# Kernel tuning notes

Hardware: AMD Instinct MI355X
Metric: run time of the kernel (lower is better)

The kernel has to match this reference:

```python
import jax, jax.numpy as jnp
import numpy as np

DIM = 2048
DIM_HEAD = 64
HEADS = 16
FF_MULT = 4
LORA_R = 8
ATTN_INNER = DIM_HEAD * HEADS            # 1024
FF_INNER = DIM * FF_MULT                 # 8192
FUSED_DIMS = (ATTN_INNER, DIM_HEAD, DIM_HEAD, FF_INNER * 2)
B, N = 2, 2048


def setup_inputs() -> dict:
    key = jax.random.key(0)
    ks = jax.random.split(key, 12)
    s = 0.02
    inp = {
        "x": jax.random.normal(ks[0], (B, N, DIM), dtype=jnp.float32),
        "gamma": jnp.ones((DIM,), dtype=jnp.float32),
        "w_fused": jax.random.normal(ks[1], (DIM, sum(FUSED_DIMS)), dtype=jnp.float32) * s,
        "w_attn_out": jax.random.normal(ks[2], (ATTN_INNER, DIM), dtype=jnp.float32) * s,
        "w_ff_out": jax.random.normal(ks[3], (FF_INNER, DIM), dtype=jnp.float32) * s,
        "lora_q_a": jax.random.normal(ks[4], (DIM, LORA_R), dtype=jnp.float32) * s,
        "lora_q_b": jax.random.normal(ks[5], (LORA_R, ATTN_INNER), dtype=jnp.float32) * s,
        "lora_k_a": jax.random.normal(ks[6], (DIM, LORA_R), dtype=jnp.float32) * s,
        "lora_k_b": jax.random.normal(ks[7], (LORA_R, DIM_HEAD), dtype=jnp.float32) * s,
        "lora_v_a": jax.random.normal(ks[8], (DIM, LORA_R), dtype=jnp.float32) * s,
        "lora_v_b": jax.random.normal(ks[9], (LORA_R, DIM_HEAD), dtype=jnp.float32) * s,
        "lora_o_a": jax.random.normal(ks[10], (ATTN_INNER, LORA_R), dtype=jnp.float32) * s,
        "lora_o_b": jax.random.normal(ks[11], (LORA_R, DIM), dtype=jnp.float32) * s,
    }
    return inp


def _rotate_half(x):
    x1, x2 = jnp.split(x, 2, axis=-1)
    return jnp.concatenate((-x2, x1), axis=-1)


def _rope(pos, t):
    return t * jnp.cos(pos) + _rotate_half(t) * jnp.sin(pos)


def _forward(x, gamma, w_fused, w_attn_out, w_ff_out,
             lora_q_a, lora_q_b, lora_k_a, lora_k_b,
             lora_v_a, lora_v_b, lora_o_a, lora_o_b):
    b, n, d = x.shape
    # LayerNorm (beta = 0)
    mu = jnp.mean(x, axis=-1, keepdims=True)
    var = jnp.var(x, axis=-1, keepdims=True)
    xn = (x - mu) * jax.lax.rsqrt(var + 1e-5) * gamma

    fused = xn @ w_fused
    i0, i1, i2 = np.cumsum(FUSED_DIMS)[:3]
    q, k, v, ff = fused[..., :i0], fused[..., i0:i1], fused[..., i1:i2], fused[..., i2:]

    # LoRA additive terms
    q = q + (xn @ lora_q_a) @ lora_q_b
    k = k + (xn @ lora_k_a) @ lora_k_b
    v = v + (xn @ lora_v_a) @ lora_v_b

    q = q.reshape(b, n, HEADS, DIM_HEAD).transpose(0, 2, 1, 3)  # b h n d
    q = q * (DIM_HEAD ** -0.5)

    # rotary embedding: pos (n, dim_head)
    inv_freq = 1.0 / (10000.0 ** (jnp.arange(0, DIM_HEAD, 2, dtype=jnp.float32) / DIM_HEAD))
    freqs = jnp.arange(n, dtype=jnp.float32)[:, None] * inv_freq[None, :]
    pos = jnp.concatenate((freqs, freqs), axis=-1)
    q = _rope(pos, q)
    k = _rope(pos, k)  # k is b n d (multi-query, single kv head)

    sim = jnp.einsum('bhid,bjd->bhij', q, k)
    causal = jnp.triu(jnp.ones((n, n), dtype=bool), k=1)
    sim = jnp.where(causal, -jnp.finfo(sim.dtype).max, sim)
    attn = jax.nn.softmax(sim, axis=-1)
    out = jnp.einsum('bhij,bjd->bhid', attn, v)
    out = out.transpose(0, 2, 1, 3).reshape(b, n, ATTN_INNER)

    attn_out = out @ w_attn_out + (out @ lora_o_a) @ lora_o_b

    # SwiGLU: chunk -> (x_ff, gate); silu(gate) * x_ff
    x_ff, gate = jnp.split(ff, 2, axis=-1)
    ff_out = (jax.nn.silu(gate) * x_ff) @ w_ff_out

    return attn_out + ff_out


def reference(x, gamma, w_fused, w_attn_out, w_ff_out,
              lora_q_a, lora_q_b, lora_k_a, lora_k_b,
              lora_v_a, lora_v_b, lora_o_a, lora_o_b):
    return _forward(x, gamma, w_fused, w_attn_out, w_ff_out,
                    lora_q_a, lora_q_b, lora_k_a, lora_k_b,
                    lora_v_a, lora_v_b, lora_o_a, lora_o_b)
```

## Files before the change

### kernel.cpp

```cpp
#include <hip/hip_runtime.h>
#include <cstdint>


typedef __bf16 bf16_t;
typedef __bf16 bf16x8 __attribute__((ext_vector_type(8)));
typedef float f32x4 __attribute__((ext_vector_type(4)));

#define LOG2E 1.44269504088896340736f

__device__ __forceinline__ void gload_lds16(const void* g, void* l) {
  __builtin_amdgcn_global_load_lds(
      (__attribute__((address_space(1))) void*)(uintptr_t)g,
      (__attribute__((address_space(3))) void*)(uint32_t)(uintptr_t)l,
      16, 0, 0);
}

__device__ __forceinline__ f32x4 mfma16(bf16x8 a, bf16x8 b, f32x4 c) {
  return __builtin_amdgcn_mfma_f32_16x16x32_bf16(a, b, c, 0, 0, 0);
}

__global__ __launch_bounds__(256) void ln_kernel(
    const float* __restrict__ x, const float* __restrict__ gamma,
    bf16_t* __restrict__ xn)
{
  const int row = blockIdx.x;
  const int t = threadIdx.x;
  const float4* xr = (const float4*)(x + (size_t)row * 2048);
  float4 a = xr[t * 2];
  float4 b = xr[t * 2 + 1];
  float s  = a.x + a.y + a.z + a.w + b.x + b.y + b.z + b.w;
  float ss = a.x*a.x + a.y*a.y + a.z*a.z + a.w*a.w
           + b.x*b.x + b.y*b.y + b.z*b.z + b.w*b.w;
  #pragma unroll
  for (int m = 1; m < 64; m <<= 1) {
    s  += __shfl_xor(s, m);
    ss += __shfl_xor(ss, m);
  }
  __shared__ float red[8];
  const int wave = t >> 6, lane = t & 63;
  if (lane == 0) { red[wave] = s; red[4 + wave] = ss; }
  __syncthreads();
  const float stot  = red[0] + red[1] + red[2] + red[3];
  const float sstot = red[4] + red[5] + red[6] + red[7];
  const float mu  = stot * (1.f / 2048.f);
  const float var = sstot * (1.f / 2048.f) - mu * mu;
  const float rs  = rsqrtf(var + 1e-5f);
  float v[8] = {a.x, a.y, a.z, a.w, b.x, b.y, b.z, b.w};
  bf16x8 o;
  #pragma unroll
  for (int e = 0; e < 8; ++e)
    o[e] = (bf16_t)((v[e] - mu) * rs * gamma[t * 8 + e]);
  *(bf16x8*)(xn + (size_t)row * 2048 + t * 8) = o;
}

__global__ __launch_bounds__(256) void transpose_wf_kernel(
    const float* __restrict__ w,
    const float* __restrict__ qa, const float* __restrict__ qb,
    const float* __restrict__ ka, const float* __restrict__ kb,
    const float* __restrict__ va, const float* __restrict__ vb,
    bf16_t* __restrict__ wfT)
{
  __shared__ float tile[64][65];
  const int t  = threadIdx.x;
  const int n0 = blockIdx.x * 64;
  const int k0 = blockIdx.y * 64;
  #pragma unroll
  for (int it = 0; it < 4; ++it) {
    const int kr = (t >> 4) + it * 16;
    const float4 vv = *(const float4*)(w + (size_t)(k0 + kr) * 17536 + n0 + (t & 15) * 4);
    tile[kr][(t & 15) * 4 + 0] = vv.x;
    tile[kr][(t & 15) * 4 + 1] = vv.y;
    tile[kr][(t & 15) * 4 + 2] = vv.z;
    tile[kr][(t & 15) * 4 + 3] = vv.w;
  }
  __syncthreads();
  const float* la = nullptr; const float* lb = nullptr;
  int nbo = 0, ldlb = 0;
  if (n0 < 1024)      { la = qa; lb = qb; nbo = n0;        ldlb = 1024; }
  else if (n0 < 1088) { la = ka; lb = kb; nbo = n0 - 1024; ldlb = 64;   }
  else if (n0 < 1152) { la = va; lb = vb; nbo = n0 - 1088; ldlb = 64;   }
  #pragma unroll
  for (int it = 0; it < 2; ++it) {
    const int nl = (t >> 3) + it * 32;
    const int kl = (t & 7) * 8;
    float vals[8];
    #pragma unroll
    for (int e = 0; e < 8; ++e) vals[e] = tile[kl + e][nl];
    if (la) {
      float bc[8];
      #pragma unroll
      for (int r = 0; r < 8; ++r) bc[r] = lb[r * ldlb + nbo + nl];
      #pragma unroll
      for (int e = 0; e < 8; ++e) {
        const float* ar = la + (size_t)(k0 + kl + e) * 8;
        float d = 0.f;
        #pragma unroll
        for (int r = 0; r < 8; ++r) d += ar[r] * bc[r];
        vals[e] += d;
      }
    }
    bf16x8 o;
    #pragma unroll
    for (int e = 0; e < 8; ++e) o[e] = (bf16_t)vals[e];
    *(bf16x8*)(wfT + (size_t)(n0 + nl) * 2048 + k0 + kl) = o;
  }
}

__global__ __launch_bounds__(256) void transpose_w2_kernel(
    const float* __restrict__ wff,
    const float* __restrict__ watt,
    const float* __restrict__ oa, const float* __restrict__ ob,
    bf16_t* __restrict__ w2T)
{
  __shared__ float tile[64][65];
  const int t  = threadIdx.x;
  const int n0 = blockIdx.x * 64;
  const int k0 = blockIdx.y * 64;
  const bool isatt = (k0 >= 8192);
  const float* src = isatt ? (watt + (size_t)(k0 - 8192) * 2048)
                           : (wff + (size_t)k0 * 2048);
  #pragma unroll
  for (int it = 0; it < 4; ++it) {
    const int kr = (t >> 4) + it * 16;
    const float4 vv = *(const float4*)(src + (size_t)kr * 2048 + n0 + (t & 15) * 4);
    tile[kr][(t & 15) * 4 + 0] = vv.x;
    tile[kr][(t & 15) * 4 + 1] = vv.y;
    tile[kr][(t & 15) * 4 + 2] = vv.z;
    tile[kr][(t & 15) * 4 + 3] = vv.w;
  }
  __syncthreads();
  #pragma unroll
  for (int it = 0; it < 2; ++it) {
    const int nl = (t >> 3) + it * 32;
    const int kl = (t & 7) * 8;
    float vals[8];
    #pragma unroll
    for (int e = 0; e < 8; ++e) vals[e] = tile[kl + e][nl];
    if (isatt) {
      float bc[8];
      #pragma unroll
      for (int r = 0; r < 8; ++r) bc[r] = ob[r * 2048 + n0 + nl];
      #pragma unroll
      for (int e = 0; e < 8; ++e) {
        const float* ar = oa + (size_t)(k0 - 8192 + kl + e) * 8;
        float d = 0.f;
        #pragma unroll
        for (int r = 0; r < 8; ++r) d += ar[r] * bc[r];
        vals[e] += d;
      }
    }
    bf16x8 o;
    #pragma unroll
    for (int e = 0; e < 8; ++e) o[e] = (bf16_t)vals[e];
    *(bf16x8*)(w2T + (size_t)(n0 + nl) * 9216 + k0 + kl) = o;
  }
}

__device__ __forceinline__ void gemm_core_128x128(
    const bf16_t* __restrict__ A, int ldA, int m0,
    const bf16_t* __restrict__ BT, int ldB, int n0,
    int K, bf16_t* As, bf16_t* Bs, f32x4* acc)
{
  const int t = threadIdx.x;
  const int wave = t >> 6;
  const int lane = t & 63;
  const int quad = lane >> 4;
  const int ln15 = lane & 15;
  const int wm = wave & 1, wn = wave >> 1;

  const bf16_t* gA = A + (size_t)(m0 + (t >> 2)) * ldA + ((t & 3) << 3);
  const bf16_t* gB = BT + (size_t)(n0 + (t >> 2)) * ldB + ((t & 3) << 3);
  char* lA = (char*)As + wave * 1024;
  char* lB = (char*)Bs + wave * 1024;
  const size_t sA64 = (size_t)64 * ldA;
  const size_t sB64 = (size_t)64 * ldB;
  const int aoff = (wm * 64 + ln15) * 32 + quad * 8;
  const int boff = (wn * 64 + ln15) * 32 + quad * 8;

  for (int kt = 0; kt < K; kt += 32) {
    gload_lds16(gA,        lA);
    gload_lds16(gA + sA64, lA + 4096);
    gload_lds16(gB,        lB);
    gload_lds16(gB + sB64, lB + 4096);
    gA += 32;
    gB += 32;
    __syncthreads();
    bf16x8 a0 = *(const bf16x8*)(As + aoff);
    bf16x8 a1 = *(const bf16x8*)(As + aoff + 512);
    bf16x8 a2 = *(const bf16x8*)(As + aoff + 1024);
    bf16x8 a3 = *(const bf16x8*)(As + aoff + 1536);
    bf16x8 b0 = *(const bf16x8*)(Bs + boff);
    bf16x8 b1 = *(const bf16x8*)(Bs + boff + 512);
    bf16x8 b2 = *(const bf16x8*)(Bs + boff + 1024);
    bf16x8 b3 = *(const bf16x8*)(Bs + boff + 1536);
    acc[0]  = mfma16(a0, b0, acc[0]);
    acc[1]  = mfma16(a0, b1, acc[1]);
    acc[2]  = mfma16(a0, b2, acc[2]);
    acc[3]  = mfma16(a0, b3, acc[3]);
    acc[4]  = mfma16(a1, b0, acc[4]);
    acc[5]  = mfma16(a1, b1, acc[5]);
    acc[6]  = mfma16(a1, b2, acc[6]);
    acc[7]  = mfma16(a1, b3, acc[7]);
    acc[8]  = mfma16(a2, b0, acc[8]);
    acc[9]  = mfma16(a2, b1, acc[9]);
    acc[10] = mfma16(a2, b2, acc[10]);
    acc[11] = mfma16(a2, b3, acc[11]);
    acc[12] = mfma16(a3, b0, acc[12]);
    acc[13] = mfma16(a3, b1, acc[13]);
    acc[14] = mfma16(a3, b2, acc[14]);
    acc[15] = mfma16(a3, b3, acc[15]);
    __syncthreads();
  }
}

__global__ __launch_bounds__(256) void gemm1_qkv_kernel(
    const bf16_t* __restrict__ xn, const bf16_t* __restrict__ wfT,
    float* __restrict__ qkv)
{
  __shared__ __align__(16) bf16_t As[128 * 32];
  __shared__ __align__(16) bf16_t Bs[128 * 32];
  const int m0 = blockIdx.x * 128;
  const int ct = blockIdx.y;
  const int t = threadIdx.x;
  const int wave = t >> 6, lane = t & 63;
  const int quad = lane >> 4, ln15 = lane & 15;
  const int wm = wave & 1, wn = wave >> 1;

  f32x4 acc[16];
  #pragma unroll
  for (int f = 0; f < 16; ++f) acc[f] = (f32x4){0.f, 0.f, 0.f, 0.f};
  gemm_core_128x128(xn, 2048, m0, wfT, 2048, ct * 128, 2048, As, Bs, acc);
  const int rb = m0 + wm * 64 + quad * 4;
  const int cb = ct * 128 + wn * 64 + ln15;
  #pragma unroll
  for (int i = 0; i < 4; ++i)
    #pragma unroll
    for (int rr = 0; rr < 4; ++rr) {
      float* dst = qkv + (size_t)(rb + i * 16 + rr) * 1152 + cb;
      #pragma unroll
      for (int j = 0; j < 4; ++j) dst[j * 16] = acc[i * 4 + j][rr];
    }
}

__global__ __launch_bounds__(256, 2) void gemm1_ff_kernel(
    const bf16_t* __restrict__ xn, const bf16_t* __restrict__ wfT,
    bf16_t* __restrict__ A2)
{
  __shared__ __align__(16) bf16_t As[128 * 32];
  __shared__ __align__(16) bf16_t Bg[128 * 32];
  __shared__ __align__(16) bf16_t Bx[128 * 32];
  const int m0 = blockIdx.x * 128;
  const int c  = blockIdx.y;
  const int t = threadIdx.x;
  const int wave = t >> 6, lane = t & 63;
  const int quad = lane >> 4, ln15 = lane & 15;
  const int wm = wave & 1, wn = wave >> 1;

  const bf16_t* gA = xn  + (size_t)(m0 + (t >> 2)) * 2048 + ((t & 3) << 3);
  const bf16_t* gG = wfT + (size_t)(9344 + c * 128 + (t >> 2)) * 2048 + ((t & 3) << 3);
  const bf16_t* gX = wfT + (size_t)(1152 + c * 128 + (t >> 2)) * 2048 + ((t & 3) << 3);
  char* lA = (char*)As + wave * 1024;
  char* lG = (char*)Bg + wave * 1024;
  char* lX = (char*)Bx + wave * 1024;
  const size_t s64 = (size_t)64 * 2048;
  const int aoff = (wm * 64 + ln15) * 32 + quad * 8;
  const int boff = (wn * 64 + ln15) * 32 + quad * 8;

  f32x4 accg[16], accx[16];
  #pragma unroll
  for (int f = 0; f < 16; ++f) {
    accg[f] = (f32x4){0.f, 0.f, 0.f, 0.f};
    accx[f] = (f32x4){0.f, 0.f, 0.f, 0.f};
  }

  for (int kt = 0; kt < 2048; kt += 32) {
    gload_lds16(gA,       lA);
    gload_lds16(gA + s64, lA + 4096);
    gload_lds16(gG,       lG);
    gload_lds16(gG + s64, lG + 4096);
    gload_lds16(gX,       lX);
    gload_lds16(gX + s64, lX + 4096);
    gA += 32; gG += 32; gX += 32;
    __syncthreads();
    bf16x8 a0 = *(const bf16x8*)(As + aoff);
    bf16x8 a1 = *(const bf16x8*)(As + aoff + 512);
    bf16x8 a2 = *(const bf16x8*)(As + aoff + 1024);
    bf16x8 a3 = *(const bf16x8*)(As + aoff + 1536);
    bf16x8 g0 = *(const bf16x8*)(Bg + boff);
    bf16x8 g1 = *(const bf16x8*)(Bg + boff + 512);
    bf16x8 g2 = *(const bf16x8*)(Bg + boff + 1024);
    bf16x8 g3 = *(const bf16x8*)(Bg + boff + 1536);
    bf16x8 x0 = *(const bf16x8*)(Bx + boff);
    bf16x8 x1 = *(const bf16x8*)(Bx + boff + 512);
    bf16x8 x2 = *(const bf16x8*)(Bx + boff + 1024);
    bf16x8 x3 = *(const bf16x8*)(Bx + boff + 1536);
    accg[0]  = mfma16(a0, g0, accg[0]);
    accg[1]  = mfma16(a0, g1, accg[1]);
    accg[2]  = mfma16(a0, g2, accg[2]);
    accg[3]  = mfma16(a0, g3, accg[3]);
    accx[0]  = mfma16(a0, x0, accx[0]);
    accx[1]  = mfma16(a0, x1, accx[1]);
    accx[2]  = mfma16(a0, x2, accx[2]);
    accx[3]  = mfma16(a0, x3, accx[3]);
    accg[4]  = mfma16(a1, g0, accg[4]);
    accg[5]  = mfma16(a1, g1, accg[5]);
    accg[6]  = mfma16(a1, g2, accg[6]);
    accg[7]  = mfma16(a1, g3, accg[7]);
    accx[4]  = mfma16(a1, x0, accx[4]);
    accx[5]  = mfma16(a1, x1, accx[5]);
    accx[6]  = mfma16(a1, x2, accx[6]);
    accx[7]  = mfma16(a1, x3, accx[7]);
    accg[8]  = mfma16(a2, g0, accg[8]);
    accg[9]  = mfma16(a2, g1, accg[9]);
    accg[10] = mfma16(a2, g2, accg[10]);
    accg[11] = mfma16(a2, g3, accg[11]);
    accx[8]  = mfma16(a2, x0, accx[8]);
    accx[9]  = mfma16(a2, x1, accx[9]);
    accx[10] = mfma16(a2, x2, accx[10]);
    accx[11] = mfma16(a2, x3, accx[11]);
    accg[12] = mfma16(a3, g0, accg[12]);
    accg[13] = mfma16(a3, g1, accg[13]);
    accg[14] = mfma16(a3, g2, accg[14]);
    accg[15] = mfma16(a3, g3, accg[15]);
    accx[12] = mfma16(a3, x0, accx[12]);
    accx[13] = mfma16(a3, x1, accx[13]);
    accx[14] = mfma16(a3, x2, accx[14]);
    accx[15] = mfma16(a3, x3, accx[15]);
    __syncthreads();
  }

  const int rb = m0 + wm * 64 + quad * 4;
  const int cb = c * 128 + wn * 64 + ln15;
  #pragma unroll
  for (int i = 0; i < 4; ++i)
    #pragma unroll
    for (int rr = 0; rr < 4; ++rr) {
      bf16_t* dst = A2 + (size_t)(rb + i * 16 + rr) * 9216 + cb;
      #pragma unroll
      for (int j = 0; j < 4; ++j) {
        const float g = accg[i * 4 + j][rr];
        const float xv = accx[i * 4 + j][rr];
        dst[j * 16] = (bf16_t)(xv * (g / (1.f + exp2f(-g * LOG2E))));
      }
    }
}

__global__ __launch_bounds__(256) void gemm2_kernel(
    const bf16_t* __restrict__ A2, const bf16_t* __restrict__ w2T,
    float* __restrict__ out)
{
  __shared__ __align__(16) bf16_t As[128 * 32];
  __shared__ __align__(16) bf16_t Bs[128 * 32];
  const int m0 = blockIdx.x * 128;
  const int n0 = blockIdx.y * 128;
  const int t = threadIdx.x;
  const int wave = t >> 6, lane = t & 63;
  const int quad = lane >> 4, ln15 = lane & 15;
  const int wm = wave & 1, wn = wave >> 1;

  f32x4 acc[16];
  #pragma unroll
  for (int f = 0; f < 16; ++f) acc[f] = (f32x4){0.f, 0.f, 0.f, 0.f};
  gemm_core_128x128(A2, 9216, m0, w2T, 9216, n0, 9216, As, Bs, acc);
  const int rb = m0 + wm * 64 + quad * 4;
  const int cb = n0 + wn * 64 + ln15;
  #pragma unroll
  for (int i = 0; i < 4; ++i)
    #pragma unroll
    for (int rr = 0; rr < 4; ++rr) {
      float* dst = out + (size_t)(rb + i * 16 + rr) * 2048 + cb;
      #pragma unroll
      for (int j = 0; j < 4; ++j) dst[j * 16] = acc[i * 4 + j][rr];
    }
}

__global__ __launch_bounds__(256) void qkv_prep_kernel(
    const float* __restrict__ qkv, bf16_t* __restrict__ Q,
    bf16_t* __restrict__ K, bf16_t* __restrict__ Vt)
{
  const int row = blockIdx.x;
  const int t = threadIdx.x;
  const int b = row >> 11, n = row & 2047;
  __shared__ float buf[1152];
  const float4* src4 = (const float4*)(qkv + (size_t)row * 1152);
  for (int i = t; i < 288; i += 256) ((float4*)buf)[i] = src4[i];
  __syncthreads();

  const float fn = (float)n;
  #pragma unroll
  for (int u = 0; u < 4; ++u) {
    const int e = t * 4 + u;
    const int hd = e >> 6, d = e & 63;
    const float val = buf[e];
    const float rot = (d < 32) ? -buf[hd * 64 + d + 32] : buf[hd * 64 + d - 32];
    const int dm = d & 31;
    const float invf = exp2f(-(float)dm * (13.287712379549449f / 32.0f));
    const float ang = fn * invf;
    float c, s;
    sincosf(ang, &s, &c);
    const float o = (val * c + rot * s) * 0.125f;
    Q[(((size_t)b * 16 + hd) * 2048 + n) * 64 + d] = (bf16_t)o;
  }
  if (t < 64) {
    const int d = t;
    const float val = buf[1024 + d];
    const float rot = (d < 32) ? -buf[1024 + d + 32] : buf[1024 + d - 32];
    const int dm = d & 31;
    const float invf = exp2f(-(float)dm * (13.287712379549449f / 32.0f));
    const float ang = fn * invf;
    float c, s;
    sincosf(ang, &s, &c);
    K[((size_t)b * 2048 + n) * 64 + d] = (bf16_t)(val * c + rot * s);
    Vt[((size_t)b * 64 + d) * 2048 + n] = (bf16_t)buf[1088 + d];
  }
}

__global__ __launch_bounds__(256) void attn_kernel(
    const bf16_t* __restrict__ Q, const bf16_t* __restrict__ Kg_,
    const bf16_t* __restrict__ Vt, bf16_t* __restrict__ A2)
{
  __shared__ __align__(16) bf16_t Qs[128 * 64];
  __shared__ __align__(16) bf16_t Ks[64 * 64];
  __shared__ __align__(16) bf16_t Vs[64 * 64];
  __shared__ __align__(16) bf16_t Ps[128 * 64];
  const int qt = blockIdx.x, bh = blockIdx.y;
  const int b = bh >> 4, h = bh & 15;
  const int qm0 = qt * 128;
  const int t = threadIdx.x;
  const int wave = t >> 6, lane = t & 63;
  const int quad = lane >> 4, ln15 = lane & 15;

  const bf16_t* Qg = Q + ((size_t)bh * 2048 + qm0) * 64;
  const bf16_t* Kg = Kg_ + (size_t)b * 2048 * 64;
  const bf16_t* Vg = Vt + (size_t)b * 64 * 2048;

  {
    const bf16_t* g = Qg + (size_t)(t >> 3) * 64 + ((t & 7) << 3);
    char* l = (char*)Qs + wave * 1024;
    gload_lds16(g,            l);
    gload_lds16(g + 32 * 64,  l + 4096);
    gload_lds16(g + 64 * 64,  l + 8192);
    gload_lds16(g + 96 * 64,  l + 12288);
  }

  float mstate[2][4], lstate[2][4];
  f32x4 o_acc[2][4];
  #pragma unroll
  for (int i = 0; i < 2; ++i)
    #pragma unroll
    for (int rr = 0; rr < 4; ++rr) { mstate[i][rr] = -1e30f; lstate[i][rr] = 0.f; }
  #pragma unroll
  for (int i = 0; i < 2; ++i)
    #pragma unroll
    for (int jd = 0; jd < 4; ++jd) o_acc[i][jd] = (f32x4){0.f, 0.f, 0.f, 0.f};

  const int njt = qt * 2 + 2;
  for (int jt = 0; jt < njt; ++jt) {
    {
      const bf16_t* kg = Kg + (size_t)(jt * 64 + (t >> 3)) * 64 + ((t & 7) << 3);
      char* lk = (char*)Ks + wave * 1024;
      gload_lds16(kg,           lk);
      gload_lds16(kg + 32 * 64, lk + 4096);
      const bf16_t* vg = Vg + (size_t)(t >> 3) * 2048 + jt * 64 + ((t & 7) << 3);
      char* lv = (char*)Vs + wave * 1024;
      gload_lds16(vg,                   lv);
      gload_lds16(vg + (size_t)32*2048, lv + 4096);
    }
    __syncthreads();

    f32x4 sA[2][4];
    #pragma unroll
    for (int i = 0; i < 2; ++i)
      #pragma unroll
      for (int j = 0; j < 4; ++j) sA[i][j] = (f32x4){0.f, 0.f, 0.f, 0.f};
    #pragma unroll
    for (int ks = 0; ks < 2; ++ks) {
      bf16x8 aq0 = *(const bf16x8*)(Qs + (wave * 32 + ln15) * 64 + ks * 32 + quad * 8);
      bf16x8 aq1 = *(const bf16x8*)(Qs + (wave * 32 + 16 + ln15) * 64 + ks * 32 + quad * 8);
      #pragma unroll
      for (int j = 0; j < 4; ++j) {
        bf16x8 bk = *(const bf16x8*)(Ks + (j * 16 + ln15) * 64 + ks * 32 + quad * 8);
        sA[0][j] = mfma16(aq0, bk, sA[0][j]);
        sA[1][j] = mfma16(aq1, bk, sA[1][j]);
      }
    }

    const bool needmask = (jt * 64 + 63 > qm0 + wave * 32);
    #pragma unroll
    for (int i = 0; i < 2; ++i) {
      const int row0 = qm0 + wave * 32 + i * 16 + quad * 4;
      float alpha[4];
      #pragma unroll
      for (int rr = 0; rr < 4; ++rr) {
        const int rowg = row0 + rr;
        if (needmask) {
          #pragma unroll
          for (int j = 0; j < 4; ++j) {
            const int colg = jt * 64 + j * 16 + ln15;
            if (colg > rowg) sA[i][j][rr] = -1e30f;
          }
        }
        float mx = fmaxf(fmaxf(sA[i][0][rr], sA[i][1][rr]),
                         fmaxf(sA[i][2][rr], sA[i][3][rr]));
        mx = fmaxf(mx, __shfl_xor(mx, 1));
        mx = fmaxf(mx, __shfl_xor(mx, 2));
        mx = fmaxf(mx, __shfl_xor(mx, 4));
        mx = fmaxf(mx, __shfl_xor(mx, 8));
        const float mold = mstate[i][rr];
        const float mnew = fmaxf(mold, mx);
        const float al = exp2f((mold - mnew) * LOG2E);
        float rsum = 0.f;
        #pragma unroll
        for (int j = 0; j < 4; ++j) {
          const float p = exp2f((sA[i][j][rr] - mnew) * LOG2E);
          sA[i][j][rr] = p;
          rsum += p;
        }
        rsum += __shfl_xor(rsum, 1);
        rsum += __shfl_xor(rsum, 2);
        rsum += __shfl_xor(rsum, 4);
        rsum += __shfl_xor(rsum, 8);
        lstate[i][rr] = lstate[i][rr] * al + rsum;
        mstate[i][rr] = mnew;
        alpha[rr] = al;
      }
      #pragma unroll
      for (int jd = 0; jd < 4; ++jd)
        #pragma unroll
        for (int rr = 0; rr < 4; ++rr)
          o_acc[i][jd][rr] *= alpha[rr];
      #pragma unroll
      for (int j = 0; j < 4; ++j)
        #pragma unroll
        for (int rr = 0; rr < 4; ++rr)
          Ps[wave * 2048 + (i * 16 + quad * 4 + rr) * 64 + j * 16 + ln15] =
              (bf16_t)sA[i][j][rr];
    }

    #pragma unroll
    for (int ks = 0; ks < 2; ++ks) {
      bf16x8 ap0 = *(const bf16x8*)(Ps + wave * 2048 + ln15 * 64 + ks * 32 + quad * 8);
      bf16x8 ap1 = *(const bf16x8*)(Ps + wave * 2048 + (16 + ln15) * 64 + ks * 32 + quad * 8);
      #pragma unroll
      for (int jd = 0; jd < 4; ++jd) {
        bf16x8 bv = *(const bf16x8*)(Vs + (jd * 16 + ln15) * 64 + ks * 32 + quad * 8);
        o_acc[0][jd] = mfma16(ap0, bv, o_acc[0][jd]);
        o_acc[1][jd] = mfma16(ap1, bv, o_acc[1][jd]);
      }
    }
    __syncthreads();
  }

  #pragma unroll
  for (int i = 0; i < 2; ++i) {
    const int row0 = qm0 + wave * 32 + i * 16 + quad * 4;
    #pragma unroll
    for (int rr = 0; rr < 4; ++rr) {
      const float inv = 1.f / lstate[i][rr];
      bf16_t* dst = A2 + ((size_t)b * 2048 + row0 + rr) * 9216 + 8192 + h * 64 + ln15;
      #pragma unroll
      for (int jd = 0; jd < 4; ++jd)
        dst[jd * 16] = (bf16_t)(o_acc[i][jd][rr] * inv);
    }
  }
}

extern "C" void kernel_launch(void* const* d_in, const int* in_sizes, int n_in,
                              void* d_out, int out_size, void* d_ws, size_t ws_size,
                              hipStream_t stream)
{
  const float* x      = (const float*)d_in[0];
  const float* gamma  = (const float*)d_in[1];
  const float* wfused = (const float*)d_in[2];
  const float* watt   = (const float*)d_in[3];
  const float* wff    = (const float*)d_in[4];
  const float* qa     = (const float*)d_in[5];
  const float* qb     = (const float*)d_in[6];
  const float* ka     = (const float*)d_in[7];
  const float* kb     = (const float*)d_in[8];
  const float* va     = (const float*)d_in[9];
  const float* vb     = (const float*)d_in[10];
  const float* oa     = (const float*)d_in[11];
  const float* ob     = (const float*)d_in[12];
  float* out = (float*)d_out;

  char* ws = (char*)d_ws;
  bf16_t* xn  = (bf16_t*)(ws);
  bf16_t* wfT = (bf16_t*)(ws + 16777216);
  bf16_t* w2T = (bf16_t*)(ws + 88604672);
  float*  qkv = (float*)(ws + 126353408);
  bf16_t* A2  = (bf16_t*)(ws + 145227776);
  bf16_t* Qr  = (bf16_t*)(ws + 220725248);
  bf16_t* Kr  = (bf16_t*)(ws + 229113856);
  bf16_t* Vtr = (bf16_t*)(ws + 229638144);

  ln_kernel<<<dim3(4096), dim3(256), 0, stream>>>(x, gamma, xn);
  transpose_wf_kernel<<<dim3(274, 32), dim3(256), 0, stream>>>(
      wfused, qa, qb, ka, kb, va, vb, wfT);
  transpose_w2_kernel<<<dim3(32, 144), dim3(256), 0, stream>>>(
      wff, watt, oa, ob, w2T);
  gemm1_qkv_kernel<<<dim3(32, 9), dim3(256), 0, stream>>>(xn, wfT, qkv);
  gemm1_ff_kernel<<<dim3(32, 64), dim3(256), 0, stream>>>(xn, wfT, A2);
  qkv_prep_kernel<<<dim3(4096), dim3(256), 0, stream>>>(qkv, Qr, Kr, Vtr);
  attn_kernel<<<dim3(16, 32), dim3(256), 0, stream>>>(Qr, Kr, Vtr, A2);
  gemm2_kernel<<<dim3(32, 16), dim3(256), 0, stream>>>(A2, w2T, out);
}
```

Baseline: 1.058 ms.

## Fuse RoPE into QKV GEMM, balance causal attention, split-K output GEMM

The QKV GEMM epilogue now applies RoPE, the 1/8 query scaling and the V transpose directly, so the fp32 qkv buffer and the separate prep kernel are gone. The attention kernel pairs query tiles qt and 15-qt in one block so each block gets the same amount of causal work. The output GEMM switches to 128x256 tiles with split-K over two halves, accumulates via atomic adds into a zeroed output, and the memset adds an extra pass. Atomics make the final sum order nondeterministic, and the larger accumulator set raises register pressure.

```diff
diff --git a/kernel.cpp b/kernel.cpp
--- a/kernel.cpp
+++ b/kernel.cpp
@@ -7,6 +7,7 @@
 typedef float f32x4 __attribute__((ext_vector_type(4)));
 
 #define LOG2E 1.44269504088896340736f
+#define LOG2_10K 13.287712379549449f
 
 __device__ __forceinline__ void gload_lds16(const void* g, void* l) {
   __builtin_amdgcn_global_load_lds(
@@ -215,7 +216,7 @@
 
 __global__ __launch_bounds__(256) void gemm1_qkv_kernel(
     const bf16_t* __restrict__ xn, const bf16_t* __restrict__ wfT,
-    float* __restrict__ qkv)
+    bf16_t* __restrict__ Q, bf16_t* __restrict__ K, bf16_t* __restrict__ Vt)
 {
   __shared__ __align__(16) bf16_t As[128 * 32];
   __shared__ __align__(16) bf16_t Bs[128 * 32];
@@ -230,16 +231,47 @@
   #pragma unroll
   for (int f = 0; f < 16; ++f) acc[f] = (f32x4){0.f, 0.f, 0.f, 0.f};
   gemm_core_128x128(xn, 2048, m0, wfT, 2048, ct * 128, 2048, As, Bs, acc);
+
   const int rb = m0 + wm * 64 + quad * 4;
-  const int cb = ct * 128 + wn * 64 + ln15;
-  #pragma unroll
-  for (int i = 0; i < 4; ++i)
+  const bool is_k = (ct == 8) && (wn == 0);
+  const bool is_v = (ct == 8) && (wn == 1);
+  const float invf0 = exp2f(-(float)ln15 * (LOG2_10K / 32.0f));
+  const float invf1 = exp2f(-(float)(16 + ln15) * (LOG2_10K / 32.0f));
+  const int hd = ct * 2 + wn;
+
+  #pragma unroll
+  for (int i = 0; i < 4; ++i) {
     #pragma unroll
     for (int rr = 0; rr < 4; ++rr) {
-      float* dst = qkv + (size_t)(rb + i * 16 + rr) * 1152 + cb;
-      #pragma unroll
-      for (int j = 0; j < 4; ++j) dst[j * 16] = acc[i * 4 + j][rr];
+      const int row = rb + i * 16 + rr;
+      const int b = row >> 11, n = row & 2047;
+      float vals[4];
+      #pragma unroll
+      for (int j = 0; j < 4; ++j) vals[j] = acc[i * 4 + j][rr];
+      if (is_v) {
+        #pragma unroll
+        for (int j = 0; j < 4; ++j)
+          Vt[((size_t)b * 64 + j * 16 + ln15) * 2048 + n] = (bf16_t)vals[j];
+      } else {
+        const float fn = (float)n;
+        float s0, c0, s1, c1;
+        __sincosf(fn * invf0, &s0, &c0);
+        __sincosf(fn * invf1, &s1, &c1);
+        #pragma unroll
+        for (int j = 0; j < 4; ++j) {
+          const float rot = (j < 2) ? -vals[j + 2] : vals[j - 2];
+          const float c = (j & 1) ? c1 : c0;
+          const float s = (j & 1) ? s1 : s0;
+          const float o = vals[j] * c + rot * s;
+          const int d = j * 16 + ln15;
+          if (is_k)
+            K[((size_t)b * 2048 + n) * 64 + d] = (bf16_t)o;
+          else
+            Q[(((size_t)b * 16 + hd) * 2048 + n) * 64 + d] = (bf16_t)(o * 0.125f);
+        }
+      }
     }
+  }
 }
 
 __global__ __launch_bounds__(256, 2) void gemm1_ff_kernel(
@@ -345,73 +377,108 @@
     }
 }
 
-__global__ __launch_bounds__(256) void gemm2_kernel(
+__global__ __launch_bounds__(256, 2) void gemm2_kernel(
     const bf16_t* __restrict__ A2, const bf16_t* __restrict__ w2T,
     float* __restrict__ out)
 {
   __shared__ __align__(16) bf16_t As[128 * 32];
-  __shared__ __align__(16) bf16_t Bs[128 * 32];
+  __shared__ __align__(16) bf16_t B0[128 * 32];
+  __shared__ __align__(16) bf16_t B1[128 * 32];
   const int m0 = blockIdx.x * 128;
-  const int n0 = blockIdx.y * 128;
+  const int n0 = blockIdx.y * 256;
+  const int k0 = blockIdx.z * 4608;
   const int t = threadIdx.x;
   const int wave = t >> 6, lane = t & 63;
   const int quad = lane >> 4, ln15 = lane & 15;
   const int wm = wave & 1, wn = wave >> 1;
 
-  f32x4 acc[16];
-  #pragma unroll
-  for (int f = 0; f < 16; ++f) acc[f] = (f32x4){0.f, 0.f, 0.f, 0.f};
-  gemm_core_128x128(A2, 9216, m0, w2T, 9216, n0, 9216, As, Bs, acc);
+  const bf16_t* gA  = A2  + (size_t)(m0 + (t >> 2)) * 9216 + k0 + ((t & 3) << 3);
+  const bf16_t* gB0 = w2T + (size_t)(n0 + (t >> 2)) * 9216 + k0 + ((t & 3) << 3);
+  const bf16_t* gB1 = w2T + (size_t)(n0 + 128 + (t >> 2)) * 9216 + k0 + ((t & 3) << 3);
+  char* lA = (char*)As + wave * 1024;
+  char* l0 = (char*)B0 + wave * 1024;
+  char* l1 = (char*)B1 + wave * 1024;
+  const size_t s64 = (size_t)64 * 9216;
+  const int aoff = (wm * 64 + ln15) * 32 + quad * 8;
+  const int boff = (wn * 64 + ln15) * 32 + quad * 8;
+
+  f32x4 acc0[16], acc1[16];
+  #pragma unroll
+  for (int f = 0; f < 16; ++f) {
+    acc0[f] = (f32x4){0.f, 0.f, 0.f, 0.f};
+    acc1[f] = (f32x4){0.f, 0.f, 0.f, 0.f};
+  }
+
+  for (int kt = 0; kt < 4608; kt += 32) {
+    gload_lds16(gA,        lA);
+    gload_lds16(gA + s64,  lA + 4096);
+    gload_lds16(gB0,       l0);
+    gload_lds16(gB0 + s64, l0 + 4096);
+    gload_lds16(gB1,       l1);
+    gload_lds16(gB1 + s64, l1 + 4096);
+    gA += 32; gB0 += 32; gB1 += 32;
+    __syncthreads();
+    bf16x8 a0 = *(const bf16x8*)(As + aoff);
+    bf16x8 a1 = *(const bf16x8*)(As + aoff + 512);
+    bf16x8 a2 = *(const bf16x8*)(As + aoff + 1024);
+    bf16x8 a3 = *(const bf16x8*)(As + aoff + 1536);
+    bf16x8 p0 = *(const bf16x8*)(B0 + boff);
+    bf16x8 p1 = *(const bf16x8*)(B0 + boff + 512);
+    bf16x8 p2 = *(const bf16x8*)(B0 + boff + 1024);
+    bf16x8 p3 = *(const bf16x8*)(B0 + boff + 1536);
+    bf16x8 q0 = *(const bf16x8*)(B1 + boff);
+    bf16x8 q1 = *(const bf16x8*)(B1 + boff + 512);
+    bf16x8 q2 = *(const bf16x8*)(B1 + boff + 1024);
+    bf16x8 q3 = *(const bf16x8*)(B1 + boff + 1536);
+    acc0[0]  = mfma16(a0, p0, acc0[0]);
+    acc0[1]  = mfma16(a0, p1, acc0[1]);
+    acc0[2]  = mfma16(a0, p2, acc0[2]);
+    acc0[3]  = mfma16(a0, p3, acc0[3]);
+    acc1[0]  = mfma16(a0, q0, acc1[0]);
+    acc1[1]  = mfma16(a0, q1, acc1[1]);
+    acc1[2]  = mfma16(a0, q2, acc1[2]);
+    acc1[3]  = mfma16(a0, q3, acc1[3]);
+    acc0[4]  = mfma16(a1, p0, acc0[4]);
+    acc0[5]  = mfma16(a1, p1, acc0[5]);
+    acc0[6]  = mfma16(a1, p2, acc0[6]);
+    acc0[7]  = mfma16(a1, p3, acc0[7]);
+    acc1[4]  = mfma16(a1, q0, acc1[4]);
+    acc1[5]  = mfma16(a1, q1, acc1[5]);
+    acc1[6]  = mfma16(a1, q2, acc1[6]);
+    acc1[7]  = mfma16(a1, q3, acc1[7]);
+    acc0[8]  = mfma16(a2, p0, acc0[8]);
+    acc0[9]  = mfma16(a2, p1, acc0[9]);
+    acc0[10] = mfma16(a2, p2, acc0[10]);
+    acc0[11] = mfma16(a2, p3, acc0[11]);
+    acc1[8]  = mfma16(a2, q0, acc1[8]);
+    acc1[9]  = mfma16(a2, q1, acc1[9]);
+    acc1[10] = mfma16(a2, q2, acc1[10]);
+    acc1[11] = mfma16(a2, q3, acc1[11]);
+    acc0[12] = mfma16(a3, p0, acc0[12]);
+    acc0[13] = mfma16(a3, p1, acc0[13]);
+    acc0[14] = mfma16(a3, p2, acc0[14]);
+    acc0[15] = mfma16(a3, p3, acc0[15]);
+    acc1[12] = mfma16(a3, q0, acc1[12]);
+    acc1[13] = mfma16(a3, q1, acc1[13]);
+    acc1[14] = mfma16(a3, q2, acc1[14]);
+    acc1[15] = mfma16(a3, q3, acc1[15]);
+    __syncthreads();
+  }
+
   const int rb = m0 + wm * 64 + quad * 4;
-  const int cb = n0 + wn * 64 + ln15;
-  #pragma unroll
-  for (int i = 0; i < 4; ++i)
-    #pragma unroll
-    for (int rr = 0; rr < 4; ++rr) {
-      float* dst = out + (size_t)(rb + i * 16 + rr) * 2048 + cb;
-      #pragma unroll
-      for (int j = 0; j < 4; ++j) dst[j * 16] = acc[i * 4 + j][rr];
-    }
-}
-
-__global__ __launch_bounds__(256) void qkv_prep_kernel(
-    const float* __restrict__ qkv, bf16_t* __restrict__ Q,
-    bf16_t* __restrict__ K, bf16_t* __restrict__ Vt)
-{
-  const int row = blockIdx.x;
-  const int t = threadIdx.x;
-  const int b = row >> 11, n = row & 2047;
-  __shared__ float buf[1152];
-  const float4* src4 = (const float4*)(qkv + (size_t)row * 1152);
-  for (int i = t; i < 288; i += 256) ((float4*)buf)[i] = src4[i];
-  __syncthreads();
-
-  const float fn = (float)n;
-  #pragma unroll
-  for (int u = 0; u < 4; ++u) {
-    const int e = t * 4 + u;
-    const int hd = e >> 6, d = e & 63;
-    const float val = buf[e];
-    const float rot = (d < 32) ? -buf[hd * 64 + d + 32] : buf[hd * 64 + d - 32];
-    const int dm = d & 31;
-    const float invf = exp2f(-(float)dm * (13.287712379549449f / 32.0f));
-    const float ang = fn * invf;
-    float c, s;
-    sincosf(ang, &s, &c);
-    const float o = (val * c + rot * s) * 0.125f;
-    Q[(((size_t)b * 16 + hd) * 2048 + n) * 64 + d] = (bf16_t)o;
-  }
-  if (t < 64) {
-    const int d = t;
-    const float val = buf[1024 + d];
-    const float rot = (d < 32) ? -buf[1024 + d + 32] : buf[1024 + d - 32];
-    const int dm = d & 31;
-    const float invf = exp2f(-(float)dm * (13.287712379549449f / 32.0f));
-    const float ang = fn * invf;
-    float c, s;
-    sincosf(ang, &s, &c);
-    K[((size_t)b * 2048 + n) * 64 + d] = (bf16_t)(val * c + rot * s);
-    Vt[((size_t)b * 64 + d) * 2048 + n] = (bf16_t)buf[1088 + d];
+  #pragma unroll
+  for (int half = 0; half < 2; ++half) {
+    const f32x4* acc = half ? acc1 : acc0;
+    const int cb = n0 + half * 128 + wn * 64 + ln15;
+    #pragma unroll
+    for (int i = 0; i < 4; ++i)
+      #pragma unroll
+      for (int rr = 0; rr < 4; ++rr) {
+        float* dst = out + (size_t)(rb + i * 16 + rr) * 2048 + cb;
+        #pragma unroll
+        for (int j = 0; j < 4; ++j)
+          unsafeAtomicAdd(dst + j * 16, acc[i * 4 + j][rr]);
+      }
   }
 }
 
@@ -423,144 +490,148 @@
   __shared__ __align__(16) bf16_t Ks[64 * 64];
   __shared__ __align__(16) bf16_t Vs[64 * 64];
   __shared__ __align__(16) bf16_t Ps[128 * 64];
-  const int qt = blockIdx.x, bh = blockIdx.y;
+  const int pidx = blockIdx.x, bh = blockIdx.y;
   const int b = bh >> 4, h = bh & 15;
-  const int qm0 = qt * 128;
   const int t = threadIdx.x;
   const int wave = t >> 6, lane = t & 63;
   const int quad = lane >> 4, ln15 = lane & 15;
 
-  const bf16_t* Qg = Q + ((size_t)bh * 2048 + qm0) * 64;
   const bf16_t* Kg = Kg_ + (size_t)b * 2048 * 64;
   const bf16_t* Vg = Vt + (size_t)b * 64 * 2048;
 
-  {
-    const bf16_t* g = Qg + (size_t)(t >> 3) * 64 + ((t & 7) << 3);
-    char* l = (char*)Qs + wave * 1024;
-    gload_lds16(g,            l);
-    gload_lds16(g + 32 * 64,  l + 4096);
-    gload_lds16(g + 64 * 64,  l + 8192);
-    gload_lds16(g + 96 * 64,  l + 12288);
-  }
-
-  float mstate[2][4], lstate[2][4];
-  f32x4 o_acc[2][4];
-  #pragma unroll
-  for (int i = 0; i < 2; ++i)
-    #pragma unroll
-    for (int rr = 0; rr < 4; ++rr) { mstate[i][rr] = -1e30f; lstate[i][rr] = 0.f; }
-  #pragma unroll
-  for (int i = 0; i < 2; ++i)
-    #pragma unroll
-    for (int jd = 0; jd < 4; ++jd) o_acc[i][jd] = (f32x4){0.f, 0.f, 0.f, 0.f};
-
-  const int njt = qt * 2 + 2;
-  for (int jt = 0; jt < njt; ++jt) {
+  for (int hlf = 0; hlf < 2; ++hlf) {
+    const int qt = hlf ? (15 - pidx) : pidx;
+    const int qm0 = qt * 128;
+    const bf16_t* Qg = Q + ((size_t)bh * 2048 + qm0) * 64;
+
     {
-      const bf16_t* kg = Kg + (size_t)(jt * 64 + (t >> 3)) * 64 + ((t & 7) << 3);
-      char* lk = (char*)Ks + wave * 1024;
-      gload_lds16(kg,           lk);
-      gload_lds16(kg + 32 * 64, lk + 4096);
-      const bf16_t* vg = Vg + (size_t)(t >> 3) * 2048 + jt * 64 + ((t & 7) << 3);
-      char* lv = (char*)Vs + wave * 1024;
-      gload_lds16(vg,                   lv);
-      gload_lds16(vg + (size_t)32*2048, lv + 4096);
+      const bf16_t* g = Qg + (size_t)(t >> 3) * 64 + ((t & 7) << 3);
+      char* l = (char*)Qs + wave * 1024;
+      gload_lds16(g,            l);
+      gload_lds16(g + 32 * 64,  l + 4096);
+      gload_lds16(g + 64 * 64,  l + 8192);
+      gload_lds16(g + 96 * 64,  l + 12288);
     }
-    __syncthreads();
-
-    f32x4 sA[2][4];
+
+    float mstate[2][4], lstate[2][4];
+    f32x4 o_acc[2][4];
     #pragma unroll
     for (int i = 0; i < 2; ++i)
       #pragma unroll
-      for (int j = 0; j < 4; ++j) sA[i][j] = (f32x4){0.f, 0.f, 0.f, 0.f};
-    #pragma unroll
-    for (int ks = 0; ks < 2; ++ks) {
-      bf16x8 aq0 = *(const bf16x8*)(Qs + (wave * 32 + ln15) * 64 + ks * 32 + quad * 8);
-      bf16x8 aq1 = *(const bf16x8*)(Qs + (wave * 32 + 16 + ln15) * 64 + ks * 32 + quad * 8);
-      #pragma unroll
-      for (int j = 0; j < 4; ++j) {
-        bf16x8 bk = *(const bf16x8*)(Ks + (j * 16 + ln15) * 64 + ks * 32 + quad * 8);
-        sA[0][j] = mfma16(aq0, bk, sA[0][j]);
-        sA[1][j] = mfma16(aq1, bk, sA[1][j]);
-      }
+      for (int rr = 0; rr < 4; ++rr) { mstate[i][rr] = -1e30f; lstate[i][rr] = 0.f; }
+    #pragma unroll
+    for (int i = 0; i < 2; ++i)
+      #pragma unroll
+      for (int jd = 0; jd < 4; ++jd) o_acc[i][jd] = (f32x4){0.f, 0.f, 0.f, 0.f};
+
+    const int njt = qt * 2 + 2;
+    for (int jt = 0; jt < njt; ++jt) {
+      {
+        const bf16_t* kg = Kg + (size_t)(jt * 64 + (t >> 3)) * 64 + ((t & 7) << 3);
+        char* lk = (char*)Ks + wave * 1024;
+        gload_lds16(kg,           lk);
+        gload_lds16(kg + 32 * 64, lk + 4096);
+        const bf16_t* vg = Vg + (size_t)(t >> 3) * 2048 + jt * 64 + ((t & 7) << 3);
+        char* lv = (char*)Vs + wave * 1024;
+        gload_lds16(vg,                   lv);
+        gload_lds16(vg + (size_t)32*2048, lv + 4096);
+      }
+      __syncthreads();
+
+      f32x4 sA[2][4];
+      #pragma unroll
+      for (int i = 0; i < 2; ++i)
+        #pragma unroll
+        for (int j = 0; j < 4; ++j) sA[i][j] = (f32x4){0.f, 0.f, 0.f, 0.f};
+      #pragma unroll
+      for (int ks = 0; ks < 2; ++ks) {
+        bf16x8 aq0 = *(const bf16x8*)(Qs + (wave * 32 + ln15) * 64 + ks * 32 + quad * 8);
+        bf16x8 aq1 = *(const bf16x8*)(Qs + (wave * 32 + 16 + ln15) * 64 + ks * 32 + quad * 8);
+        #pragma unroll
+        for (int j = 0; j < 4; ++j) {
+          bf16x8 bk = *(const bf16x8*)(Ks + (j * 16 + ln15) * 64 + ks * 32 + quad * 8);
+          sA[0][j] = mfma16(aq0, bk, sA[0][j]);
+          sA[1][j] = mfma16(aq1, bk, sA[1][j]);
+        }
+      }
+
+      const bool needmask = (jt * 64 + 63 > qm0 + wave * 32);
+      #pragma unroll
+      for (int i = 0; i < 2; ++i) {
+        const int row0 = qm0 + wave * 32 + i * 16 + quad * 4;
+        float alpha[4];
+        #pragma unroll
+        for (int rr = 0; rr < 4; ++rr) {
+          const int rowg = row0 + rr;
+          if (needmask) {
+            #pragma unroll
+            for (int j = 0; j < 4; ++j) {
+              const int colg = jt * 64 + j * 16 + ln15;
+              if (colg > rowg) sA[i][j][rr] = -1e30f;
+            }
+          }
+          float mx = fmaxf(fmaxf(sA[i][0][rr], sA[i][1][rr]),
+                           fmaxf(sA[i][2][rr], sA[i][3][rr]));
+          mx = fmaxf(mx, __shfl_xor(mx, 1));
+          mx = fmaxf(mx, __shfl_xor(mx, 2));
+          mx = fmaxf(mx, __shfl_xor(mx, 4));
+          mx = fmaxf(mx, __shfl_xor(mx, 8));
+          const float mold = mstate[i][rr];
+          const float mnew = fmaxf(mold, mx);
+          const float al = exp2f((mold - mnew) * LOG2E);
+          float rsum = 0.f;
+          #pragma unroll
+          for (int j = 0; j < 4; ++j) {
+            const float p = exp2f((sA[i][j][rr] - mnew) * LOG2E);
+            sA[i][j][rr] = p;
+            rsum += p;
+          }
+          rsum += __shfl_xor(rsum, 1);
+          rsum += __shfl_xor(rsum, 2);
+          rsum += __shfl_xor(rsum, 4);
+          rsum += __shfl_xor(rsum, 8);
+          lstate[i][rr] = lstate[i][rr] * al + rsum;
+          mstate[i][rr] = mnew;
+          alpha[rr] = al;
+        }
+        #pragma unroll
+        for (int jd = 0; jd < 4; ++jd)
+          #pragma unroll
+          for (int rr = 0; rr < 4; ++rr)
+            o_acc[i][jd][rr] *= alpha[rr];
+        #pragma unroll
+        for (int j = 0; j < 4; ++j)
+          #pragma unroll
+          for (int rr = 0; rr < 4; ++rr)
+            Ps[wave * 2048 + (i * 16 + quad * 4 + rr) * 64 + j * 16 + ln15] =
+                (bf16_t)sA[i][j][rr];
+      }
+
+      #pragma unroll
+      for (int ks = 0; ks < 2; ++ks) {
+        bf16x8 ap0 = *(const bf16x8*)(Ps + wave * 2048 + ln15 * 64 + ks * 32 + quad * 8);
+        bf16x8 ap1 = *(const bf16x8*)(Ps + wave * 2048 + (16 + ln15) * 64 + ks * 32 + quad * 8);
+        #pragma unroll
+        for (int jd = 0; jd < 4; ++jd) {
+          bf16x8 bv = *(const bf16x8*)(Vs + (jd * 16 + ln15) * 64 + ks * 32 + quad * 8);
+          o_acc[0][jd] = mfma16(ap0, bv, o_acc[0][jd]);
+          o_acc[1][jd] = mfma16(ap1, bv, o_acc[1][jd]);
+        }
+      }
+      __syncthreads();
     }
 
-    const bool needmask = (jt * 64 + 63 > qm0 + wave * 32);
     #pragma unroll
     for (int i = 0; i < 2; ++i) {
       const int row0 = qm0 + wave * 32 + i * 16 + quad * 4;
-      float alpha[4];
       #pragma unroll
       for (int rr = 0; rr < 4; ++rr) {
-        const int rowg = row0 + rr;
-        if (needmask) {
-          #pragma unroll
-          for (int j = 0; j < 4; ++j) {
-            const int colg = jt * 64 + j * 16 + ln15;
-            if (colg > rowg) sA[i][j][rr] = -1e30f;
-          }
-        }
-        float mx = fmaxf(fmaxf(sA[i][0][rr], sA[i][1][rr]),
-                         fmaxf(sA[i][2][rr], sA[i][3][rr]));
-        mx = fmaxf(mx, __shfl_xor(mx, 1));
-        mx = fmaxf(mx, __shfl_xor(mx, 2));
-        mx = fmaxf(mx, __shfl_xor(mx, 4));
-        mx = fmaxf(mx, __shfl_xor(mx, 8));
-        const float mold = mstate[i][rr];
-        const float mnew = fmaxf(mold, mx);
-        const float al = exp2f((mold - mnew) * LOG2E);
-        float rsum = 0.f;
-        #pragma unroll
-        for (int j = 0; j < 4; ++j) {
-          const float p = exp2f((sA[i][j][rr] - mnew) * LOG2E);
-          sA[i][j][rr] = p;
-          rsum += p;
-        }
-        rsum += __shfl_xor(rsum, 1);
-        rsum += __shfl_xor(rsum, 2);
-        rsum += __shfl_xor(rsum, 4);
-        rsum += __shfl_xor(rsum, 8);
-        lstate[i][rr] = lstate[i][rr] * al + rsum;
-        mstate[i][rr] = mnew;
-        alpha[rr] = al;
-      }
-      #pragma unroll
-      for (int jd = 0; jd < 4; ++jd)
-        #pragma unroll
-        for (int rr = 0; rr < 4; ++rr)
-          o_acc[i][jd][rr] *= alpha[rr];
-      #pragma unroll
-      for (int j = 0; j < 4; ++j)
-        #pragma unroll
-        for (int rr = 0; rr < 4; ++rr)
-          Ps[wave * 2048 + (i * 16 + quad * 4 + rr) * 64 + j * 16 + ln15] =
-              (bf16_t)sA[i][j][rr];
-    }
-
-    #pragma unroll
-    for (int ks = 0; ks < 2; ++ks) {
-      bf16x8 ap0 = *(const bf16x8*)(Ps + wave * 2048 + ln15 * 64 + ks * 32 + quad * 8);
-      bf16x8 ap1 = *(const bf16x8*)(Ps + wave * 2048 + (16 + ln15) * 64 + ks * 32 + quad * 8);
-      #pragma unroll
-      for (int jd = 0; jd < 4; ++jd) {
-        bf16x8 bv = *(const bf16x8*)(Vs + (jd * 16 + ln15) * 64 + ks * 32 + quad * 8);
-        o_acc[0][jd] = mfma16(ap0, bv, o_acc[0][jd]);
-        o_acc[1][jd] = mfma16(ap1, bv, o_acc[1][jd]);
-      }
-    }
-    __syncthreads();
-  }
-
-  #pragma unroll
-  for (int i = 0; i < 2; ++i) {
-    const int row0 = qm0 + wave * 32 + i * 16 + quad * 4;
-    #pragma unroll
-    for (int rr = 0; rr < 4; ++rr) {
-      const float inv = 1.f / lstate[i][rr];
-      bf16_t* dst = A2 + ((size_t)b * 2048 + row0 + rr) * 9216 + 8192 + h * 64 + ln15;
-      #pragma unroll
-      for (int jd = 0; jd < 4; ++jd)
-        dst[jd * 16] = (bf16_t)(o_acc[i][jd][rr] * inv);
+        const float inv = 1.f / lstate[i][rr];
+        bf16_t* dst = A2 + ((size_t)b * 2048 + row0 + rr) * 9216 + 8192 + h * 64 + ln15;
+        #pragma unroll
+        for (int jd = 0; jd < 4; ++jd)
+          dst[jd * 16] = (bf16_t)(o_acc[i][jd][rr] * inv);
+      }
     }
   }
 }
@@ -588,20 +659,20 @@
   bf16_t* xn  = (bf16_t*)(ws);
   bf16_t* wfT = (bf16_t*)(ws + 16777216);
   bf16_t* w2T = (bf16_t*)(ws + 88604672);
-  float*  qkv = (float*)(ws + 126353408);
-  bf16_t* A2  = (bf16_t*)(ws + 145227776);
-  bf16_t* Qr  = (bf16_t*)(ws + 220725248);
-  bf16_t* Kr  = (bf16_t*)(ws + 229113856);
-  bf16_t* Vtr = (bf16_t*)(ws + 229638144);
+  bf16_t* A2  = (bf16_t*)(ws + 126353408);
+  bf16_t* Qr  = (bf16_t*)(ws + 201850880);
+  bf16_t* Kr  = (bf16_t*)(ws + 210239488);
+  bf16_t* Vtr = (bf16_t*)(ws + 210763776);
+
+  hipMemsetAsync(d_out, 0, (size_t)out_size * sizeof(float), stream);
 
   ln_kernel<<<dim3(4096), dim3(256), 0, stream>>>(x, gamma, xn);
   transpose_wf_kernel<<<dim3(274, 32), dim3(256), 0, stream>>>(
       wfused, qa, qb, ka, kb, va, vb, wfT);
   transpose_w2_kernel<<<dim3(32, 144), dim3(256), 0, stream>>>(
       wff, watt, oa, ob, w2T);
-  gemm1_qkv_kernel<<<dim3(32, 9), dim3(256), 0, stream>>>(xn, wfT, qkv);
+  gemm1_qkv_kernel<<<dim3(32, 9), dim3(256), 0, stream>>>(xn, wfT, Qr, Kr, Vtr);
   gemm1_ff_kernel<<<dim3(32, 64), dim3(256), 0, stream>>>(xn, wfT, A2);
-  qkv_prep_kernel<<<dim3(4096), dim3(256), 0, stream>>>(qkv, Qr, Kr, Vtr);
-  attn_kernel<<<dim3(16, 32), dim3(256), 0, stream>>>(Qr, Kr, Vtr, A2);
-  gemm2_kernel<<<dim3(32, 16), dim3(256), 0, stream>>>(A2, w2T, out);
-}
+  attn_kernel<<<dim3(8, 32), dim3(256), 0, stream>>>(Qr, Kr, Vtr, A2);
+  gemm2_kernel<<<dim3(32, 8, 2), dim3(256), 0, stream>>>(A2, w2T, out);
+}
```

Measured after the change: 1.010 ms. 4.5% less time.
